# Kernel optimization log

Hardware: AMD Instinct MI355X
Metric: run time of the kernel (lower is better)

Reference implementation:

```python
import jax, jax.numpy as jnp
import numpy as np

B, L, H, HS, OUT = 4, 512, 768, 64, 16  # batch, seq_len, hidden, head_size, output_size


def setup_inputs() -> dict:
    key = jax.random.key(0)
    ks = jax.random.split(key, 4)
    return {
        "x": jax.random.normal(ks[0], (B, L, H), dtype=jnp.float32),
        "Wq": jax.random.normal(ks[1], (H, HS), dtype=jnp.float32) * 0.02,
        "bq": jnp.zeros((HS,), dtype=jnp.float32),
        "Wk": jax.random.normal(ks[2], (H, HS), dtype=jnp.float32) * 0.02,
        "bk": jnp.zeros((HS,), dtype=jnp.float32),
        "Wb": jax.random.normal(ks[3], (4 * HS, OUT), dtype=jnp.float32) * 0.02,
        "bb": jnp.zeros((OUT,), dtype=jnp.float32),
    }


def _tri_indices(seq_len):
    # pair p corresponds to (start=i, end=j) with j >= i, ordered by i then j
    idx_start = np.repeat(np.arange(seq_len), np.arange(seq_len, 0, -1))
    idx_end = np.concatenate([np.arange(i, seq_len) for i in range(seq_len)])
    return idx_start, idx_end


def reference(x, Wq, bq, Wk, bk, Wb, bb):
    seq_len = x.shape[1]
    idx_start, idx_end = _tri_indices(seq_len)  # static numpy, P = L*(L+1)/2

    # Project per-token first (math-equivalent to projecting the gathered
    # pair tensors, since Linear is applied token-wise), then gather pairs.
    q = x @ Wq + bq  # [B, L, HS]
    k = x @ Wk + bk  # [B, L, HS]

    q_start = q[:, idx_start]  # query(start_token_hidden)  [B, P, HS]
    q_end = q[:, idx_end]      # query(end_token_hidden)
    k_end = k[:, idx_end]      # key(end_token_hidden) == key_start == key_end

    # entity_type_bias(cat([query_start, key_start, query_end, key_end]))
    feat = jnp.concatenate([q_start, k_end, q_end, k_end], axis=-1) @ Wb + bb  # [B, P, OUT]

    # einsum('blnh,blnh->bln') with n=1 -> per-pair dot product, broadcast over OUT
    score = jnp.einsum('bph,bph->bp', q_start, k_end)[..., None]  # [B, P, 1]
    return score + feat  # [B, P, OUT]
```

## Files before the change

kernel.cpp:

```cpp
#include <hip/hip_runtime.h>
#include <hip/hip_bf16.h>

#define Bc   4
#define Lc   512
#define Hc   768
#define HSc  64
#define OUTc 16
#define Pc   131328
#define KSEG 192
#define MTOK 8

typedef float floatx4 __attribute__((ext_vector_type(4)));


__global__ __launch_bounds__(512) void qk_proj_kernel(
    const float* __restrict__ x,
    const float* __restrict__ Wq, const float* __restrict__ bq,
    const float* __restrict__ Wk, const float* __restrict__ bk,
    const float* __restrict__ Wb, const float* __restrict__ bb,
    float* __restrict__ qws, float* __restrict__ kws,
    float* __restrict__ Aws, float* __restrict__ Ews)
{
    __shared__ float lds_p[4][MTOK][128];
    __shared__ float lds_c[MTOK][128];

    const int tid = threadIdx.x;
    const int wu  = __builtin_amdgcn_readfirstlane(tid >> 6);
    const int half = wu & 1;
    const int kseg = wu >> 1;
    const int col  = tid & 63;
    const int tok_base = blockIdx.x * MTOK;

    const float* Wp = half ? Wk : Wq;
    const float* wp = Wp + (size_t)kseg * KSEG * HSc + col;
    const float* xr = x + (size_t)tok_base * Hc + kseg * KSEG;

    float acc[MTOK];
    #pragma unroll
    for (int t = 0; t < MTOK; ++t) acc[t] = 0.f;

    float wA[16], wB[16];
    #pragma unroll
    for (int u = 0; u < 16; ++u) wA[u] = wp[u * HSc];

    #pragma unroll 1
    for (int j0 = 0; j0 < KSEG; j0 += 32) {
        #pragma unroll
        for (int u = 0; u < 16; ++u) wB[u] = wp[(j0 + 16 + u) * HSc];
        #pragma unroll
        for (int u = 0; u < 16; ++u) {
            const int jj = j0 + u;
            #pragma unroll
            for (int t = 0; t < MTOK; ++t)
                acc[t] += xr[t * Hc + jj] * wA[u];
        }
        if (j0 + 32 < KSEG) {
            #pragma unroll
            for (int u = 0; u < 16; ++u) wA[u] = wp[(j0 + 32 + u) * HSc];
        }
        #pragma unroll
        for (int u = 0; u < 16; ++u) {
            const int jj = j0 + 16 + u;
            #pragma unroll
            for (int t = 0; t < MTOK; ++t)
                acc[t] += xr[t * Hc + jj] * wB[u];
        }
    }

    const int n = half * 64 + col;
    #pragma unroll
    for (int t = 0; t < MTOK; ++t) lds_p[kseg][t][n] = acc[t];
    __syncthreads();

    #pragma unroll
    for (int i = tid; i < MTOK * 128; i += 512) {
        const int t = i >> 7;
        const int c = i & 127;
        float v = lds_p[0][t][c] + lds_p[1][t][c] + lds_p[2][t][c] + lds_p[3][t][c];
        const int cc = c & 63;
        if (c < 64) { v += bq[cc]; qws[(size_t)(tok_base + t) * HSc + cc] = v; }
        else        { v += bk[cc]; kws[(size_t)(tok_base + t) * HSc + cc] = v; }
        lds_c[t][c] = v;
    }
    __syncthreads();

    if (tid < MTOK * 32) {
        const int t = tid >> 5;
        const int c = tid & 31;
        const int tok = tok_base + t;
        const float* row = lds_c[t];
        if (c < 16) {
            float a = 0.f;
            #pragma unroll 8
            for (int h = 0; h < 64; ++h)
                a += row[h] * Wb[h * OUTc + c];
            Aws[(size_t)tok * OUTc + c] = a;
        } else {
            const int o = c - 16;
            float ev = bb[o];
            #pragma unroll 8
            for (int h = 0; h < 64; ++h) {
                ev += row[h]      * Wb[(128 + h) * OUTc + o];
                ev += row[64 + h] * (Wb[(64 + h) * OUTc + o] + Wb[(192 + h) * OUTc + o]);
            }
            Ews[(size_t)tok * OUTc + o] = ev;
        }
    }
}

__global__ __launch_bounds__(256) void pair_kernel(
    const float* __restrict__ qws, const float* __restrict__ kws,
    const float* __restrict__ Aws, const float* __restrict__ Ews,
    float* __restrict__ out)
{
    const int j = blockIdx.x;
    const int i = blockIdx.y;
    const int b = blockIdx.z;
    if (j < (i >> 2)) return;

    __shared__ alignas(16) float q_tile[16][64];
    __shared__ alignas(16) float A_tile[16][16];

    const int tid = threadIdx.x;
    const int s0 = i * 16;
    const int e0 = j * 64;

    {
        const int r = tid >> 4, c4 = tid & 15;
        ((float4*)q_tile[r])[c4] =
            ((const float4*)(qws + ((size_t)b * Lc + s0 + r) * HSc))[c4];
        if (tid < 64) {
            const int ra = tid >> 2, ca = tid & 3;
            ((float4*)A_tile[ra])[ca] =
                ((const float4*)(Aws + ((size_t)b * Lc + s0 + ra) * OUTc))[ca];
        }
    }
    __syncthreads();

    const int g = tid >> 2;
    const int l = tid & 3;
    const int e = e0 + g;

    const float4* kk = (const float4*)(kws + ((size_t)b * Lc + e) * HSc);
    const float4 kv0 = kk[l];
    const float4 kv1 = kk[4 + l];
    const float4 kv2 = kk[8 + l];
    const float4 kv3 = kk[12 + l];
    const float4 ev  = ((const float4*)(Ews + ((size_t)b * Lc + e) * OUTc))[l];

    float* ob = out + (size_t)b * Pc * OUTc;

    #pragma unroll 4
    for (int sl = 0; sl < 16; ++sl) {
        const int s = s0 + sl;
        const float4* qq = (const float4*)q_tile[sl];
        const float4 qv0 = qq[l];
        const float4 qv1 = qq[4 + l];
        const float4 qv2 = qq[8 + l];
        const float4 qv3 = qq[12 + l];

        float sc = qv0.x * kv0.x + qv0.y * kv0.y + qv0.z * kv0.z + qv0.w * kv0.w
                 + qv1.x * kv1.x + qv1.y * kv1.y + qv1.z * kv1.z + qv1.w * kv1.w
                 + qv2.x * kv2.x + qv2.y * kv2.y + qv2.z * kv2.z + qv2.w * kv2.w
                 + qv3.x * kv3.x + qv3.y * kv3.y + qv3.z * kv3.z + qv3.w * kv3.w;
        sc += __shfl_xor(sc, 1);
        sc += __shfl_xor(sc, 2);

        if (e >= s) {
            const float4 av = ((const float4*)A_tile[sl])[l];
            const int row = s * (2 * Lc + 1 - s) / 2 + (e - s);
            floatx4 r;
            r.x = av.x + ev.x + sc;
            r.y = av.y + ev.y + sc;
            r.z = av.z + ev.z + sc;
            r.w = av.w + ev.w + sc;
            __builtin_nontemporal_store(r, (floatx4*)(ob + (size_t)row * OUTc) + l);
        }
    }
}

extern "C" void kernel_launch(void* const* d_in, const int* in_sizes, int n_in,
                              void* d_out, int out_size, void* d_ws, size_t ws_size,
                              hipStream_t stream) {
    const float* x  = (const float*)d_in[0];
    const float* Wq = (const float*)d_in[1];
    const float* bq = (const float*)d_in[2];
    const float* Wk = (const float*)d_in[3];
    const float* bk = (const float*)d_in[4];
    const float* Wb = (const float*)d_in[5];
    const float* bb = (const float*)d_in[6];

    float* ws  = (float*)d_ws;
    float* qws = ws;
    float* kws = ws + 131072;
    float* Aws = ws + 262144;
    float* Ews = ws + 294912;

    qk_proj_kernel<<<dim3(256), dim3(512), 0, stream>>>(
        x, Wq, bq, Wk, bk, Wb, bb, qws, kws, Aws, Ews);
    pair_kernel<<<dim3(8, 32, 4), dim3(256), 0, stream>>>(
        qws, kws, Aws, Ews, (float*)d_out);
}
```

Before: 108.8 us.

## Move Q/K projection to bf16 MFMA GEMM with separate prep and bias kernels

Replaces the fp32 scalar Q/K projection with three kernels. The first converts x to bf16 and writes a transposed bf16 copy of Wq/Wk. The second runs the projection with 16x16x32 bf16 MFMA instructions, and a third computes the per-token A/E bias terms using Wb staged in shared memory. The goal is to use the matrix cores for the 2048x768x128 GEMM. In exchange it adds two extra kernel launches and workspace round-trips, and it lowers the projection's precision to bf16. The pair kernel's inner loop unroll also goes from 4 to 8.

```diff
diff --git a/kernel.cpp b/kernel.cpp
--- a/kernel.cpp
+++ b/kernel.cpp
@@ -7,104 +7,133 @@
 #define HSc  64
 #define OUTc 16
 #define Pc   131328
-#define KSEG 192
-#define MTOK 8
-
-typedef float floatx4 __attribute__((ext_vector_type(4)));
-
-
-__global__ __launch_bounds__(512) void qk_proj_kernel(
-    const float* __restrict__ x,
-    const float* __restrict__ Wq, const float* __restrict__ bq,
-    const float* __restrict__ Wk, const float* __restrict__ bk,
+#define NTOK 2048
+
+typedef float  floatx4 __attribute__((ext_vector_type(4)));
+typedef short  bf16x8  __attribute__((ext_vector_type(8)));
+typedef float  f32x4   __attribute__((ext_vector_type(4)));
+
+
+__device__ __forceinline__ unsigned short f2bf(float f) {
+    unsigned int u = __float_as_uint(f);
+    return (unsigned short)((u + 0x7FFFu + ((u >> 16) & 1u)) >> 16);
+}
+
+__global__ __launch_bounds__(256) void prep_kernel(
+    const float* __restrict__ x, const float* __restrict__ Wq,
+    const float* __restrict__ Wk,
+    unsigned short* __restrict__ xbf, unsigned short* __restrict__ Wt)
+{
+    const int bx  = blockIdx.x;
+    const int tid = threadIdx.x;
+    if (bx < 512) {
+        const float4* xg = (const float4*)x;
+        const int base = bx * 768;
+        #pragma unroll
+        for (int i = 0; i < 3; ++i) {
+            const int idx = base + tid + i * 256;
+            const float4 v = xg[idx];
+            ushort4 o;
+            o.x = f2bf(v.x); o.y = f2bf(v.y); o.z = f2bf(v.z); o.w = f2bf(v.w);
+            ((ushort4*)xbf)[idx] = o;
+        }
+    } else {
+        const int k0 = (bx - 512) * 16;
+        __shared__ unsigned short T[128][16];
+        const int c  = tid & 127;
+        const int kg = tid >> 7;
+        const float* Wsrc = (c < 64) ? Wq : Wk;
+        const int cc = c & 63;
+        #pragma unroll
+        for (int kk = 0; kk < 8; ++kk) {
+            const int k = k0 + kg * 8 + kk;
+            T[c][kg * 8 + kk] = f2bf(Wsrc[k * HSc + cc]);
+        }
+        __syncthreads();
+        const int n = tid >> 1;
+        const int h = tid & 1;
+        const unsigned short* src = &T[n][h * 8];
+        ushort4* dst = (ushort4*)(Wt + (size_t)n * Hc + k0 + h * 8);
+        dst[0] = make_ushort4(src[0], src[1], src[2], src[3]);
+        dst[1] = make_ushort4(src[4], src[5], src[6], src[7]);
+    }
+}
+
+__global__ __launch_bounds__(256) void gemm_kernel(
+    const unsigned short* __restrict__ xbf, const unsigned short* __restrict__ Wt,
+    const float* __restrict__ bq, const float* __restrict__ bk,
+    float* __restrict__ qws, float* __restrict__ kws)
+{
+    const int bx   = blockIdx.x;
+    const int mb   = bx >> 1;
+    const int nh   = bx & 1;
+    const int tid  = threadIdx.x;
+    const int w    = tid >> 6;
+    const int lane = tid & 63;
+    const int l15  = lane & 15;
+    const int quad = lane >> 4;
+
+    const int m0 = mb * 16;
+    const int nb = nh * 64 + w * 16;
+
+    const unsigned short* ap = xbf + (size_t)(m0 + l15) * Hc + quad * 8;
+    const unsigned short* bp = Wt  + (size_t)(nb + l15) * Hc + quad * 8;
+
+    f32x4 acc = {0.f, 0.f, 0.f, 0.f};
+    #pragma unroll
+    for (int k0 = 0; k0 < Hc; k0 += 32) {
+        const bf16x8 a = *(const bf16x8*)(ap + k0);
+        const bf16x8 b = *(const bf16x8*)(bp + k0);
+        acc = __builtin_amdgcn_mfma_f32_16x16x32_bf16(a, b, acc, 0, 0, 0);
+    }
+
+    const int  gn   = nb + l15;
+    const bool isq  = (gn < 64);
+    const int  col  = gn & 63;
+    const float bias = isq ? bq[col] : bk[col];
+    float* dst = isq ? qws : kws;
+    #pragma unroll
+    for (int r = 0; r < 4; ++r) {
+        const int tok = m0 + quad * 4 + r;
+        dst[(size_t)tok * HSc + col] = acc[r] + bias;
+    }
+}
+
+__global__ __launch_bounds__(256) void ae_kernel(
+    const float* __restrict__ qws, const float* __restrict__ kws,
     const float* __restrict__ Wb, const float* __restrict__ bb,
-    float* __restrict__ qws, float* __restrict__ kws,
     float* __restrict__ Aws, float* __restrict__ Ews)
 {
-    __shared__ float lds_p[4][MTOK][128];
-    __shared__ float lds_c[MTOK][128];
-
+    __shared__ float lWb[256 * OUTc];
+    __shared__ float lqk[8][128];
     const int tid = threadIdx.x;
-    const int wu  = __builtin_amdgcn_readfirstlane(tid >> 6);
-    const int half = wu & 1;
-    const int kseg = wu >> 1;
-    const int col  = tid & 63;
-    const int tok_base = blockIdx.x * MTOK;
-
-    const float* Wp = half ? Wk : Wq;
-    const float* wp = Wp + (size_t)kseg * KSEG * HSc + col;
-    const float* xr = x + (size_t)tok_base * Hc + kseg * KSEG;
-
-    float acc[MTOK];
+    const int tok_base = blockIdx.x * 8;
     #pragma unroll
-    for (int t = 0; t < MTOK; ++t) acc[t] = 0.f;
-
-    float wA[16], wB[16];
-    #pragma unroll
-    for (int u = 0; u < 16; ++u) wA[u] = wp[u * HSc];
-
-    #pragma unroll 1
-    for (int j0 = 0; j0 < KSEG; j0 += 32) {
-        #pragma unroll
-        for (int u = 0; u < 16; ++u) wB[u] = wp[(j0 + 16 + u) * HSc];
-        #pragma unroll
-        for (int u = 0; u < 16; ++u) {
-            const int jj = j0 + u;
-            #pragma unroll
-            for (int t = 0; t < MTOK; ++t)
-                acc[t] += xr[t * Hc + jj] * wA[u];
-        }
-        if (j0 + 32 < KSEG) {
-            #pragma unroll
-            for (int u = 0; u < 16; ++u) wA[u] = wp[(j0 + 32 + u) * HSc];
-        }
-        #pragma unroll
-        for (int u = 0; u < 16; ++u) {
-            const int jj = j0 + 16 + u;
-            #pragma unroll
-            for (int t = 0; t < MTOK; ++t)
-                acc[t] += xr[t * Hc + jj] * wB[u];
-        }
-    }
-
-    const int n = half * 64 + col;
-    #pragma unroll
-    for (int t = 0; t < MTOK; ++t) lds_p[kseg][t][n] = acc[t];
+    for (int i = 0; i < 16; ++i) lWb[tid + i * 256] = Wb[tid + i * 256];
+    for (int i = tid; i < 8 * 128; i += 256) {
+        const int t = i >> 7, c = i & 127;
+        lqk[t][c] = (c < 64) ? qws[(size_t)(tok_base + t) * HSc + c]
+                             : kws[(size_t)(tok_base + t) * HSc + (c - 64)];
+    }
     __syncthreads();
-
-    #pragma unroll
-    for (int i = tid; i < MTOK * 128; i += 512) {
-        const int t = i >> 7;
-        const int c = i & 127;
-        float v = lds_p[0][t][c] + lds_p[1][t][c] + lds_p[2][t][c] + lds_p[3][t][c];
-        const int cc = c & 63;
-        if (c < 64) { v += bq[cc]; qws[(size_t)(tok_base + t) * HSc + cc] = v; }
-        else        { v += bk[cc]; kws[(size_t)(tok_base + t) * HSc + cc] = v; }
-        lds_c[t][c] = v;
-    }
-    __syncthreads();
-
-    if (tid < MTOK * 32) {
-        const int t = tid >> 5;
-        const int c = tid & 31;
-        const int tok = tok_base + t;
-        const float* row = lds_c[t];
-        if (c < 16) {
-            float a = 0.f;
-            #pragma unroll 8
-            for (int h = 0; h < 64; ++h)
-                a += row[h] * Wb[h * OUTc + c];
-            Aws[(size_t)tok * OUTc + c] = a;
-        } else {
-            const int o = c - 16;
-            float ev = bb[o];
-            #pragma unroll 8
-            for (int h = 0; h < 64; ++h) {
-                ev += row[h]      * Wb[(128 + h) * OUTc + o];
-                ev += row[64 + h] * (Wb[(64 + h) * OUTc + o] + Wb[(192 + h) * OUTc + o]);
-            }
-            Ews[(size_t)tok * OUTc + o] = ev;
-        }
+    const int t = tid >> 5;
+    const int c = tid & 31;
+    const int tok = tok_base + t;
+    const float* row = lqk[t];
+    if (c < 16) {
+        float a = 0.f;
+        #pragma unroll 8
+        for (int h = 0; h < 64; ++h) a += row[h] * lWb[h * OUTc + c];
+        Aws[(size_t)tok * OUTc + c] = a;
+    } else {
+        const int o = c - 16;
+        float ev = bb[o];
+        #pragma unroll 8
+        for (int h = 0; h < 64; ++h) {
+            ev += row[h]      * lWb[(128 + h) * OUTc + o];
+            ev += row[64 + h] * (lWb[(64 + h) * OUTc + o] + lWb[(192 + h) * OUTc + o]);
+        }
+        Ews[(size_t)tok * OUTc + o] = ev;
     }
 }
 
@@ -150,7 +179,7 @@
 
     float* ob = out + (size_t)b * Pc * OUTc;
 
-    #pragma unroll 4
+    #pragma unroll 8
     for (int sl = 0; sl < 16; ++sl) {
         const int s = s0 + sl;
         const float4* qq = (const float4*)q_tile[sl];
@@ -195,9 +224,12 @@
     float* kws = ws + 131072;
     float* Aws = ws + 262144;
     float* Ews = ws + 294912;
-
-    qk_proj_kernel<<<dim3(256), dim3(512), 0, stream>>>(
-        x, Wq, bq, Wk, bk, Wb, bb, qws, kws, Aws, Ews);
+    unsigned short* xbf = (unsigned short*)(ws + 327680);
+    unsigned short* Wt  = xbf + (size_t)NTOK * Hc;
+
+    prep_kernel<<<dim3(560), dim3(256), 0, stream>>>(x, Wq, Wk, xbf, Wt);
+    gemm_kernel<<<dim3(256), dim3(256), 0, stream>>>(xbf, Wt, bq, bk, qws, kws);
+    ae_kernel<<<dim3(256), dim3(256), 0, stream>>>(qws, kws, Wb, bb, Aws, Ews);
     pair_kernel<<<dim3(8, 32, 4), dim3(256), 0, stream>>>(
         qws, kws, Aws, Ews, (float*)d_out);
 }
```

Measured after the change: 100.1 us, median of 2. 1.09x faster.

## Use bf16 MFMA for Q/K projection and split the bias epilogue across blocks

Applied to the files above, without the earlier changes.

Replaces the FP32 scalar projection kernel with a bf16 MFMA (16x16x32) kernel. Each block converts a 16-token x tile and chunks of Wq or Wk to bf16 in LDS, so every block handles one half (q or k). The E-term epilogue is split into separate q-side and k-side buffers that the pair kernel sums, and the pair loop unroll is raised. Converting to bf16 loses precision in q/k, and the projection is a small share of the runtime next to the output-write-bound pair kernel.

```diff
diff --git a/kernel.cpp b/kernel.cpp
--- a/kernel.cpp
+++ b/kernel.cpp
@@ -7,111 +7,135 @@
 #define HSc  64
 #define OUTc 16
 #define Pc   131328
-#define KSEG 192
-#define MTOK 8
+#define KC   128
+#define NCH  6
 
 typedef float floatx4 __attribute__((ext_vector_type(4)));
-
-
-__global__ __launch_bounds__(512) void qk_proj_kernel(
+typedef short bf16x8  __attribute__((ext_vector_type(8)));
+typedef float f32x4   __attribute__((ext_vector_type(4)));
+
+
+__device__ __forceinline__ unsigned short f2bf(float f) {
+    unsigned int u = __float_as_uint(f);
+    return (unsigned short)((u + 0x7FFFu + ((u >> 16) & 1u)) >> 16);
+}
+
+#define XPITCH 776
+#define WPITCH 136
+
+__global__ __launch_bounds__(256) void proj_kernel(
     const float* __restrict__ x,
     const float* __restrict__ Wq, const float* __restrict__ bq,
     const float* __restrict__ Wk, const float* __restrict__ bk,
     const float* __restrict__ Wb, const float* __restrict__ bb,
     float* __restrict__ qws, float* __restrict__ kws,
-    float* __restrict__ Aws, float* __restrict__ Ews)
+    float* __restrict__ Aws, float* __restrict__ Eqws, float* __restrict__ Ekws)
 {
-    __shared__ float lds_p[4][MTOK][128];
-    __shared__ float lds_c[MTOK][128];
-
-    const int tid = threadIdx.x;
-    const int wu  = __builtin_amdgcn_readfirstlane(tid >> 6);
-    const int half = wu & 1;
-    const int kseg = wu >> 1;
-    const int col  = tid & 63;
-    const int tok_base = blockIdx.x * MTOK;
-
-    const float* Wp = half ? Wk : Wq;
-    const float* wp = Wp + (size_t)kseg * KSEG * HSc + col;
-    const float* xr = x + (size_t)tok_base * Hc + kseg * KSEG;
-
-    float acc[MTOK];
+    __shared__ __align__(16) char lds_raw[16 * XPITCH * 2 + 64 * WPITCH * 2];
+    unsigned short* lx = (unsigned short*)lds_raw;
+    unsigned short* lw = (unsigned short*)(lds_raw + 16 * XPITCH * 2);
+    float* lc = (float*)(lds_raw + 16 * XPITCH * 2);
+
+    const int tid  = threadIdx.x;
+    const int bx   = blockIdx.x;
+    const int mb   = bx >> 1;
+    const int nh   = bx & 1;
+    const int m0   = mb * 16;
+    const int w    = tid >> 6;
+    const int lane = tid & 63;
+    const int l15  = lane & 15;
+    const int quad = lane >> 4;
+
+    {
+        const float4* xg = (const float4*)(x + (size_t)m0 * Hc);
+        #pragma unroll
+        for (int i = 0; i < 12; ++i) {
+            const int flat = tid + i * 256;
+            const int row  = flat / 192;
+            const int c4   = flat - row * 192;
+            const float4 v = xg[flat];
+            ushort4 o = make_ushort4(f2bf(v.x), f2bf(v.y), f2bf(v.z), f2bf(v.w));
+            *(ushort4*)&lx[row * XPITCH + c4 * 4] = o;
+        }
+    }
+
+    const float* Ws = nh ? Wk : Wq;
+    f32x4 acc = {0.f, 0.f, 0.f, 0.f};
+
+    for (int c = 0; c < NCH; ++c) {
+        const int k0 = c * KC;
+        if (c) __syncthreads();
+        #pragma unroll 4
+        for (int i = 0; i < 16; ++i) {
+            const int slot = tid + i * 256;
+            const int n  = slot & 63;
+            const int kp = slot >> 6;
+            const float w0 = Ws[(k0 + 2 * kp) * HSc + n];
+            const float w1 = Ws[(k0 + 2 * kp + 1) * HSc + n];
+            const unsigned int pk = (unsigned)f2bf(w0) | ((unsigned)f2bf(w1) << 16);
+            *(unsigned int*)&lw[n * WPITCH + 2 * kp] = pk;
+        }
+        __syncthreads();
+        #pragma unroll
+        for (int m = 0; m < 4; ++m) {
+            const int ko = m * 32 + quad * 8;
+            const bf16x8 a = *(const bf16x8*)&lx[l15 * XPITCH + k0 + ko];
+            const bf16x8 b = *(const bf16x8*)&lw[(w * 16 + l15) * WPITCH + ko];
+            acc = __builtin_amdgcn_mfma_f32_16x16x32_bf16(a, b, acc, 0, 0, 0);
+        }
+    }
+    __syncthreads();
+
+    const int gcol = w * 16 + l15;
+    const float bias = nh ? bk[gcol] : bq[gcol];
+    float* dst = nh ? kws : qws;
     #pragma unroll
-    for (int t = 0; t < MTOK; ++t) acc[t] = 0.f;
-
-    float wA[16], wB[16];
-    #pragma unroll
-    for (int u = 0; u < 16; ++u) wA[u] = wp[u * HSc];
-
-    #pragma unroll 1
-    for (int j0 = 0; j0 < KSEG; j0 += 32) {
+    for (int r = 0; r < 4; ++r) {
+        const int tl = quad * 4 + r;
+        const float v = acc[r] + bias;
+        dst[(size_t)(m0 + tl) * HSc + gcol] = v;
+        lc[tl * 64 + gcol] = v;
+    }
+    __syncthreads();
+
+    if (nh == 0) {
         #pragma unroll
-        for (int u = 0; u < 16; ++u) wB[u] = wp[(j0 + 16 + u) * HSc];
-        #pragma unroll
-        for (int u = 0; u < 16; ++u) {
-            const int jj = j0 + u;
-            #pragma unroll
-            for (int t = 0; t < MTOK; ++t)
-                acc[t] += xr[t * Hc + jj] * wA[u];
-        }
-        if (j0 + 32 < KSEG) {
-            #pragma unroll
-            for (int u = 0; u < 16; ++u) wA[u] = wp[(j0 + 32 + u) * HSc];
-        }
-        #pragma unroll
-        for (int u = 0; u < 16; ++u) {
-            const int jj = j0 + 16 + u;
-            #pragma unroll
-            for (int t = 0; t < MTOK; ++t)
-                acc[t] += xr[t * Hc + jj] * wB[u];
-        }
-    }
-
-    const int n = half * 64 + col;
-    #pragma unroll
-    for (int t = 0; t < MTOK; ++t) lds_p[kseg][t][n] = acc[t];
-    __syncthreads();
-
-    #pragma unroll
-    for (int i = tid; i < MTOK * 128; i += 512) {
-        const int t = i >> 7;
-        const int c = i & 127;
-        float v = lds_p[0][t][c] + lds_p[1][t][c] + lds_p[2][t][c] + lds_p[3][t][c];
-        const int cc = c & 63;
-        if (c < 64) { v += bq[cc]; qws[(size_t)(tok_base + t) * HSc + cc] = v; }
-        else        { v += bk[cc]; kws[(size_t)(tok_base + t) * HSc + cc] = v; }
-        lds_c[t][c] = v;
-    }
-    __syncthreads();
-
-    if (tid < MTOK * 32) {
-        const int t = tid >> 5;
-        const int c = tid & 31;
-        const int tok = tok_base + t;
-        const float* row = lds_c[t];
-        if (c < 16) {
-            float a = 0.f;
-            #pragma unroll 8
-            for (int h = 0; h < 64; ++h)
-                a += row[h] * Wb[h * OUTc + c];
-            Aws[(size_t)tok * OUTc + c] = a;
-        } else {
-            const int o = c - 16;
-            float ev = bb[o];
-            #pragma unroll 8
-            for (int h = 0; h < 64; ++h) {
-                ev += row[h]      * Wb[(128 + h) * OUTc + o];
-                ev += row[64 + h] * (Wb[(64 + h) * OUTc + o] + Wb[(192 + h) * OUTc + o]);
+        for (int i = 0; i < 2; ++i) {
+            const int slot = tid + i * 256;
+            const int t  = slot >> 5;
+            const int cc = slot & 31;
+            const float* row = &lc[t * 64];
+            const int tok = m0 + t;
+            if (cc < 16) {
+                float a = 0.f;
+                #pragma unroll 8
+                for (int h = 0; h < 64; ++h) a += row[h] * Wb[h * OUTc + cc];
+                Aws[(size_t)tok * OUTc + cc] = a;
+            } else {
+                const int o = cc - 16;
+                float ev = 0.f;
+                #pragma unroll 8
+                for (int h = 0; h < 64; ++h) ev += row[h] * Wb[(128 + h) * OUTc + o];
+                Eqws[(size_t)tok * OUTc + o] = ev;
             }
-            Ews[(size_t)tok * OUTc + o] = ev;
-        }
+        }
+    } else {
+        const int t = tid >> 4;
+        const int o = tid & 15;
+        const float* row = &lc[t * 64];
+        const int tok = m0 + t;
+        float ev = bb[o];
+        #pragma unroll 8
+        for (int h = 0; h < 64; ++h)
+            ev += row[h] * (Wb[(64 + h) * OUTc + o] + Wb[(192 + h) * OUTc + o]);
+        Ekws[(size_t)tok * OUTc + o] = ev;
     }
 }
 
 __global__ __launch_bounds__(256) void pair_kernel(
     const float* __restrict__ qws, const float* __restrict__ kws,
-    const float* __restrict__ Aws, const float* __restrict__ Ews,
-    float* __restrict__ out)
+    const float* __restrict__ Aws, const float* __restrict__ Eqws,
+    const float* __restrict__ Ekws, float* __restrict__ out)
 {
     const int j = blockIdx.x;
     const int i = blockIdx.y;
@@ -146,11 +170,13 @@
     const float4 kv1 = kk[4 + l];
     const float4 kv2 = kk[8 + l];
     const float4 kv3 = kk[12 + l];
-    const float4 ev  = ((const float4*)(Ews + ((size_t)b * Lc + e) * OUTc))[l];
+    const float4 e1 = ((const float4*)(Eqws + ((size_t)b * Lc + e) * OUTc))[l];
+    const float4 e2 = ((const float4*)(Ekws + ((size_t)b * Lc + e) * OUTc))[l];
+    const float4 ev = make_float4(e1.x + e2.x, e1.y + e2.y, e1.z + e2.z, e1.w + e2.w);
 
     float* ob = out + (size_t)b * Pc * OUTc;
 
-    #pragma unroll 4
+    #pragma unroll 8
     for (int sl = 0; sl < 16; ++sl) {
         const int s = s0 + sl;
         const float4* qq = (const float4*)q_tile[sl];
@@ -190,14 +216,15 @@
     const float* Wb = (const float*)d_in[5];
     const float* bb = (const float*)d_in[6];
 
-    float* ws  = (float*)d_ws;
-    float* qws = ws;
-    float* kws = ws + 131072;
-    float* Aws = ws + 262144;
-    float* Ews = ws + 294912;
-
-    qk_proj_kernel<<<dim3(256), dim3(512), 0, stream>>>(
-        x, Wq, bq, Wk, bk, Wb, bb, qws, kws, Aws, Ews);
+    float* ws   = (float*)d_ws;
+    float* qws  = ws;
+    float* kws  = ws + 131072;
+    float* Aws  = ws + 262144;
+    float* Eqws = ws + 294912;
+    float* Ekws = ws + 327680;
+
+    proj_kernel<<<dim3(256), dim3(256), 0, stream>>>(
+        x, Wq, bq, Wk, bk, Wb, bb, qws, kws, Aws, Eqws, Ekws);
     pair_kernel<<<dim3(8, 32, 4), dim3(256), 0, stream>>>(
-        qws, kws, Aws, Ews, (float*)d_out);
-}
+        qws, kws, Aws, Eqws, Ekws, (float*)d_out);
+}
```

After: 101.8 us. -6.5%, faster.
